# Performance work log

Measured on AMD Instinct MI355X. Metric: run time of the kernel, lower is better.

## Reference

```python
import jax, jax.numpy as jnp
import numpy as np

N = 50000      # nodes
E = 800000     # edges (avg degree 16)
F_IN = 256
F_OUT = 256


def setup_inputs() -> dict:
    key = jax.random.key(0)
    ks = jax.random.split(key, 8)
    feature = jax.random.normal(ks[0], (N, F_IN), dtype=jnp.float32)
    e_w = jax.random.uniform(ks[1], (E, 1), dtype=jnp.float32)
    snorm_n = jnp.ones((N, 1), dtype=jnp.float32)
    snorm_e = jnp.ones((E, 1), dtype=jnp.float32)
    src = jax.random.randint(ks[2], (E,), 0, N, dtype=jnp.int32)
    dst = jax.random.randint(ks[3], (E,), 0, N, dtype=jnp.int32)
    scale = 1.0 / np.sqrt(F_IN)
    W_self = jax.random.normal(ks[4], (F_IN, F_OUT), dtype=jnp.float32) * scale
    W = jax.random.normal(ks[5], (F_IN, F_OUT), dtype=jnp.float32) * scale
    b = jax.random.normal(ks[6], (F_OUT,), dtype=jnp.float32) * scale
    return {"feature": feature, "e_w": e_w, "snorm_n": snorm_n,
            "snorm_e": snorm_e, "W_self": W_self, "W": W, "b": b,
            "src": src, "dst": dst}


def reference(feature, e_w, snorm_n, snorm_e, W_self, W, b, src, dst):
    n = feature.shape[0]
    ones_e = jnp.ones_like(src, dtype=feature.dtype)
    # self transform
    h_s = feature @ W_self                                   # [N, F_OUT]
    # source-side degree normalization: deg_out^{-1/2}
    out_deg = jnp.maximum(jax.ops.segment_sum(ones_e, src, num_segments=n), 1.0)
    feat = feature * (out_deg ** -0.5)[:, None]              # [N, F_IN]
    # message = h[src] * e_w, aggregated by sum into dst (u_mul_e + sum reduce)
    msgs = feat[src] * e_w                                   # [E, F_IN]
    agg = jax.ops.segment_sum(msgs, dst, num_segments=n)     # [N, F_IN]
    # neighbor transform + destination-side degree normalization
    h = agg @ W + b                                          # [N, F_OUT]
    in_deg = jnp.maximum(jax.ops.segment_sum(ones_e, dst, num_segments=n), 1.0)
    h = h * (in_deg ** -0.5)[:, None]
    return h_s + h, e_w
```

## Files before the change

kernel.cpp:

```cpp
#include <hip/hip_runtime.h>
#include <hip/hip_bf16.h>

#define N_NODES 50000
#define N_EDGES 800000
#define MAXDEG  64

#define ROW_TILES    391
#define GEMM_BLOCKS  1564
#define EDGE_BLOCKS  782
#define TOTAL_BLOCKS 2346
#define WCONV_BLOCKS 512

typedef __bf16 bf16x8_t __attribute__((ext_vector_type(8)));
typedef float  f32x4_t  __attribute__((ext_vector_type(4)));

__device__ __forceinline__ unsigned short f2bf(float x) {
  __hip_bfloat16 h = __float2bfloat16(x);
  return __builtin_bit_cast(unsigned short, h);
}
__device__ __forceinline__ float bf2f(unsigned short u) {
  unsigned int v = ((unsigned int)u) << 16;
  return __builtin_bit_cast(float, v);
}
__device__ __forceinline__ unsigned int pk2(float lo, float hi) {
  return ((unsigned int)f2bf(hi) << 16) | (unsigned int)f2bf(lo);
}

__global__ __launch_bounds__(256) void wconv_kernel(
    const float* __restrict__ Wself, const float* __restrict__ W,
    unsigned short* __restrict__ Bt)
{
  int idx = blockIdx.x * 256 + threadIdx.x;
  int n = idx >> 8, k = idx & 255;
  float v = (n < 256) ? Wself[k * 256 + n] : W[k * 256 + (n - 256)];
  Bt[idx] = f2bf(v);
}

__global__ __launch_bounds__(256, 4) void gemm_edge_kernel(
    const float* __restrict__ feature,
    const unsigned short* __restrict__ Bt,
    const float* __restrict__ e_w, const int* __restrict__ src, const int* __restrict__ dst,
    int* __restrict__ cnt_in, int* __restrict__ cnt_out,
    unsigned int* __restrict__ bucket, float* __restrict__ out1,
    float* __restrict__ out0,
    unsigned char* __restrict__ y8)
{
  const int b   = blockIdx.x;
  const int tid = threadIdx.x;

  if (b % 3 == 2) {
    const int e0 = (b / 3) * 1024 + tid;
#pragma unroll
    for (int k = 0; k < 4; ++k) {
      int e = e0 + k * 256;
      if (e < N_EDGES) {
        int s = src[e];
        int d = dst[e];
        float w = e_w[e];
        out1[e] = w;
        atomicAdd(&cnt_out[s], 1);
        int p = atomicAdd(&cnt_in[d], 1);
        if (p < MAXDEG) {
          unsigned int ent = ((unsigned int)f2bf(w) << 16) | (unsigned int)s;
          bucket[(size_t)d * MAXDEG + p] = ent;
        }
      }
    }
    return;
  }

  __shared__ __align__(16) unsigned short As[2][128 * 32];
  __shared__ __align__(16) unsigned short Bs[2][128 * 32];

  const int g    = (b / 3) * 2 + (b % 3);
  const int q    = g & 3;
  const int m0   = (g >> 2) * 128;
  const int bn0  = q * 128;
  const int lane = tid & 63;
  const int wave = tid >> 6;
  const int wm   = (wave & 1) * 64;
  const int wn   = (wave >> 1) * 64;
  const int fr   = lane & 15;
  const int fkc  = lane >> 4;

  const int ra = tid >> 1, ha = tid & 1;
  const int sA = (ra >> 1) & 3;
  const int arow = (m0 + ra < N_NODES) ? (m0 + ra) : 0;
  const float* aptr = feature + (size_t)arow * 256;
  const int cg0 = (2 * ha) ^ sA;
  const int cg1 = (2 * ha + 1) ^ sA;
  const int aw0 = ra * 32 + (2 * ha) * 8;
  const int aw1 = aw0 + 8;

  f32x4_t acc[4][4] = {};

  {
#pragma unroll
    for (int i = 0; i < 2; ++i) {
      int r  = i * 64 + (tid >> 2);
      int cg = (tid & 3) ^ ((r >> 1) & 3);
      const unsigned short* gb = Bt + (size_t)(bn0 + r) * 256 + cg * 8;
      __builtin_amdgcn_global_load_lds((const __attribute__((address_space(1))) void*)gb,
                                       (__attribute__((address_space(3))) void*)&Bs[0][i * 2048 + wave * 512],
                                       16, 0, 0);
    }
    float4 a0 = *(const float4*)(aptr + cg0 * 8);
    float4 a1 = *(const float4*)(aptr + cg0 * 8 + 4);
    float4 a2 = *(const float4*)(aptr + cg1 * 8);
    float4 a3 = *(const float4*)(aptr + cg1 * 8 + 4);
    uint4 p0, p1;
    p0.x = pk2(a0.x, a0.y); p0.y = pk2(a0.z, a0.w);
    p0.z = pk2(a1.x, a1.y); p0.w = pk2(a1.z, a1.w);
    p1.x = pk2(a2.x, a2.y); p1.y = pk2(a2.z, a2.w);
    p1.z = pk2(a3.x, a3.y); p1.w = pk2(a3.z, a3.w);
    *(uint4*)&As[0][aw0] = p0;
    *(uint4*)&As[0][aw1] = p1;
  }
  __syncthreads();

#pragma unroll
  for (int s = 0; s < 8; ++s) {
    const int cb = s & 1, nb = cb ^ 1;
    float4 a0, a1, a2, a3;
    if (s < 7) {
      const int k0 = (s + 1) * 32;
#pragma unroll
      for (int i = 0; i < 2; ++i) {
        int r  = i * 64 + (tid >> 2);
        int cg = (tid & 3) ^ ((r >> 1) & 3);
        const unsigned short* gb = Bt + (size_t)(bn0 + r) * 256 + k0 + cg * 8;
        __builtin_amdgcn_global_load_lds((const __attribute__((address_space(1))) void*)gb,
                                         (__attribute__((address_space(3))) void*)&Bs[nb][i * 2048 + wave * 512],
                                         16, 0, 0);
      }
      a0 = *(const float4*)(aptr + k0 + cg0 * 8);
      a1 = *(const float4*)(aptr + k0 + cg0 * 8 + 4);
      a2 = *(const float4*)(aptr + k0 + cg1 * 8);
      a3 = *(const float4*)(aptr + k0 + cg1 * 8 + 4);
    }

    bf16x8_t af[4], bv[4];
#pragma unroll
    for (int i = 0; i < 4; ++i) {
      int R = wm + i * 16 + fr;
      af[i] = *(const bf16x8_t*)&As[cb][R * 32 + ((fkc ^ ((R >> 1) & 3)) * 8)];
    }
#pragma unroll
    for (int j = 0; j < 4; ++j) {
      int R = wn + j * 16 + fr;
      bv[j] = *(const bf16x8_t*)&Bs[cb][R * 32 + ((fkc ^ ((R >> 1) & 3)) * 8)];
    }
#pragma unroll
    for (int i = 0; i < 4; ++i)
#pragma unroll
      for (int j = 0; j < 4; ++j)
        acc[i][j] = __builtin_amdgcn_mfma_f32_16x16x32_bf16(af[i], bv[j], acc[i][j], 0, 0, 0);

    if (s < 7) {
      uint4 p0, p1;
      p0.x = pk2(a0.x, a0.y); p0.y = pk2(a0.z, a0.w);
      p0.z = pk2(a1.x, a1.y); p0.w = pk2(a1.z, a1.w);
      p1.x = pk2(a2.x, a2.y); p1.y = pk2(a2.z, a2.w);
      p1.z = pk2(a3.x, a3.y); p1.w = pk2(a3.z, a3.w);
      *(uint4*)&As[nb][aw0] = p0;
      *(uint4*)&As[nb][aw1] = p1;
      __syncthreads();
    }
  }

  if (q < 2) {
    const int cbase = q * 128 + wn + (lane & 15);
#pragma unroll
    for (int i = 0; i < 4; ++i) {
      int rowb = m0 + wm + i * 16 + (lane >> 4) * 4;
#pragma unroll
      for (int j = 0; j < 4; ++j) {
        int col = cbase + j * 16;
#pragma unroll
        for (int r = 0; r < 4; ++r) {
          int row = rowb + r;
          if (row < N_NODES)
            out0[(size_t)row * 256 + col] = acc[i][j][r];
        }
      }
    }
  } else {
    const int cbase = (q - 2) * 128 + wn + (lane & 15);
#pragma unroll
    for (int i = 0; i < 4; ++i) {
      int rowb = m0 + wm + i * 16 + (lane >> 4) * 4;
#pragma unroll
      for (int j = 0; j < 4; ++j) {
        int col = cbase + j * 16;
#pragma unroll
        for (int r = 0; r < 4; ++r) {
          int row = rowb + r;
          if (row < N_NODES) {
            float ys = acc[i][j][r];
            unsigned int pk = (unsigned int)__builtin_amdgcn_cvt_pk_fp8_f32(ys, ys, 0, false);
            y8[(size_t)row * 256 + col] = (unsigned char)(pk & 0xffu);
          }
        }
      }
    }
  }
}

__global__ __launch_bounds__(256) void agg_kernel(
    const unsigned char* __restrict__ y8, const unsigned int* __restrict__ bucket,
    const int* __restrict__ cnt_in, const int* __restrict__ cnt_out,
    const float* __restrict__ bias, float* __restrict__ out0)
{
  const int hw   = threadIdx.x >> 5;
  const int lane = threadIdx.x & 31;
  const int node = blockIdx.x * 8 + hw;
  if (node >= N_NODES) return;
  int deg_raw = cnt_in[node];
  int deg = deg_raw > MAXDEG ? MAXDEG : deg_raw;

  float a0 = 0.f, a1 = 0.f, a2 = 0.f, a3 = 0.f;
  float a4 = 0.f, a5 = 0.f, a6 = 0.f, a7 = 0.f;

  for (int bb = 0; bb < MAXDEG; bb += 32) {
    if (bb >= deg) break;
    int idx = bb + lane;
    unsigned int ent = (idx < deg) ? bucket[(size_t)node * MAXDEG + idx] : 0u;
    int   sl = (int)(ent & 0xffffu);
    float wl = bf2f((unsigned short)(ent >> 16));
    int co = cnt_out[sl]; if (co < 1) co = 1;
    wl *= rsqrtf((float)co);

#pragma unroll
    for (int t0 = 0; t0 < 32; t0 += 16) {
      if (bb + t0 >= deg) break;
#pragma unroll
      for (int t = 0; t < 16; ++t) {
        int eb = t0 + t;
        int   s = __shfl(sl, eb, 32);
        float w = __shfl(wl, eb, 32);
        uint2 u = *(const uint2*)(y8 + (size_t)s * 256 + lane * 8);
        a0 += w * __builtin_amdgcn_cvt_f32_fp8(u.x, 0);
        a1 += w * __builtin_amdgcn_cvt_f32_fp8(u.x, 1);
        a2 += w * __builtin_amdgcn_cvt_f32_fp8(u.x, 2);
        a3 += w * __builtin_amdgcn_cvt_f32_fp8(u.x, 3);
        a4 += w * __builtin_amdgcn_cvt_f32_fp8(u.y, 0);
        a5 += w * __builtin_amdgcn_cvt_f32_fp8(u.y, 1);
        a6 += w * __builtin_amdgcn_cvt_f32_fp8(u.y, 2);
        a7 += w * __builtin_amdgcn_cvt_f32_fp8(u.y, 3);
      }
    }
  }

  int dn = deg_raw < 1 ? 1 : deg_raw;
  float inv = rsqrtf((float)dn);
  float4 b0 = *(const float4*)(bias + lane * 8);
  float4 b1 = *(const float4*)(bias + lane * 8 + 4);
  size_t off = (size_t)node * 256 + lane * 8;
  float4 o0 = *(float4*)(out0 + off);
  float4 o1 = *(float4*)(out0 + off + 4);
  o0.x += (a0 + b0.x) * inv;  o0.y += (a1 + b0.y) * inv;
  o0.z += (a2 + b0.z) * inv;  o0.w += (a3 + b0.w) * inv;
  o1.x += (a4 + b1.x) * inv;  o1.y += (a5 + b1.y) * inv;
  o1.z += (a6 + b1.z) * inv;  o1.w += (a7 + b1.w) * inv;
  *(float4*)(out0 + off)     = o0;
  *(float4*)(out0 + off + 4) = o1;
}

extern "C" void kernel_launch(void* const* d_in, const int* in_sizes, int n_in,
                              void* d_out, int out_size, void* d_ws, size_t ws_size,
                              hipStream_t stream) {
  const float* feature = (const float*)d_in[0];
  const float* e_w     = (const float*)d_in[1];
  const float* W_self  = (const float*)d_in[4];
  const float* W       = (const float*)d_in[5];
  const float* bias    = (const float*)d_in[6];
  const int*   src     = (const int*)d_in[7];
  const int*   dst     = (const int*)d_in[8];

  float* out0 = (float*)d_out;
  float* out1 = out0 + (size_t)N_NODES * 256;

  char* ws = (char*)d_ws;
  int*            cnt_in  = (int*)(ws + 0);
  int*            cnt_out = (int*)(ws + 204800);
  unsigned int*   bucket  = (unsigned int*)(ws + 409600);
  unsigned short* Bt      = (unsigned short*)(ws + 13209600);
  unsigned char*  y8      = (unsigned char*)(ws + 13471744);

  hipMemsetAsync(ws, 0, 409600, stream);

  wconv_kernel<<<WCONV_BLOCKS, 256, 0, stream>>>(W_self, W, Bt);
  gemm_edge_kernel<<<TOTAL_BLOCKS, 256, 0, stream>>>(
      feature, Bt, e_w, src, dst, cnt_in, cnt_out, bucket, out1, out0, y8);
  agg_kernel<<<(N_NODES + 7) / 8, 256, 0, stream>>>(y8, bucket, cnt_in, cnt_out, bias, out0);
}
```

Before: 256.1 us.

## Replace fixed-capacity edge buckets with compact CSR built via counting and scan

Edge degree counting and rank assignment move into a prep kernel fused with the weight conversion. A single-block prefix scan then builds CSR offsets, and the edge blocks inside the GEMM kernel scatter packed entries into a compact CSR array instead of 64-slot per-node buckets. This shrinks the adjacency storage and the memset, and removes the MAXDEG truncation. The cost is an extra serial scan launch and an additional pass over the edges. The A-tile load addressing is also reworked so each thread reads contiguous global chunks and applies the swizzle on the LDS store side.

```diff
diff --git a/kernel.cpp b/kernel.cpp
--- a/kernel.cpp
+++ b/kernel.cpp
@@ -3,13 +3,12 @@
 
 #define N_NODES 50000
 #define N_EDGES 800000
-#define MAXDEG  64
 
 #define ROW_TILES    391
-#define GEMM_BLOCKS  1564
+#define WCONV_BLOCKS 512
 #define EDGE_BLOCKS  782
-#define TOTAL_BLOCKS 2346
-#define WCONV_BLOCKS 512
+#define K1_BLOCKS    (WCONV_BLOCKS + EDGE_BLOCKS)
+#define K3_BLOCKS    2346
 
 typedef __bf16 bf16x8_t __attribute__((ext_vector_type(8)));
 typedef float  f32x4_t  __attribute__((ext_vector_type(4)));
@@ -26,22 +25,69 @@
   return ((unsigned int)f2bf(hi) << 16) | (unsigned int)f2bf(lo);
 }
 
-__global__ __launch_bounds__(256) void wconv_kernel(
+__global__ __launch_bounds__(256) void prep_kernel(
     const float* __restrict__ Wself, const float* __restrict__ W,
-    unsigned short* __restrict__ Bt)
+    const float* __restrict__ e_w, const int* __restrict__ src, const int* __restrict__ dst,
+    unsigned short* __restrict__ Bt, int* __restrict__ cnt_in, int* __restrict__ cnt_out,
+    unsigned char* __restrict__ rank8, float* __restrict__ out1)
 {
-  int idx = blockIdx.x * 256 + threadIdx.x;
-  int n = idx >> 8, k = idx & 255;
-  float v = (n < 256) ? Wself[k * 256 + n] : W[k * 256 + (n - 256)];
-  Bt[idx] = f2bf(v);
+  const int b = blockIdx.x, tid = threadIdx.x;
+  if (b < WCONV_BLOCKS) {
+    int idx = b * 256 + tid;
+    int n = idx >> 8, k = idx & 255;
+    float v = (n < 256) ? Wself[k * 256 + n] : W[k * 256 + (n - 256)];
+    Bt[idx] = f2bf(v);
+    return;
+  }
+  const int e0 = (b - WCONV_BLOCKS) * 1024 + tid;
+#pragma unroll
+  for (int k = 0; k < 4; ++k) {
+    int e = e0 + k * 256;
+    if (e < N_EDGES) {
+      int s = src[e], d = dst[e];
+      out1[e] = e_w[e];
+      atomicAdd(&cnt_out[s], 1);
+      rank8[e] = (unsigned char)atomicAdd(&cnt_in[d], 1);
+    }
+  }
+}
+
+#define SCAN_CHUNK 49
+__global__ __launch_bounds__(1024) void scan_kernel(
+    const int* __restrict__ cnt, int* __restrict__ off)
+{
+  const int t = threadIdx.x;
+  const int c0 = t * SCAN_CHUNK;
+  int s = 0;
+#pragma unroll
+  for (int i = 0; i < SCAN_CHUNK; ++i) {
+    int idx = c0 + i;
+    s += (idx < N_NODES) ? cnt[idx] : 0;
+  }
+  __shared__ int sm[1024];
+  sm[t] = s;
+  __syncthreads();
+  for (int d = 1; d < 1024; d <<= 1) {
+    int v = (t >= d) ? sm[t - d] : 0;
+    __syncthreads();
+    sm[t] += v;
+    __syncthreads();
+  }
+  int run = sm[t] - s;
+#pragma unroll
+  for (int i = 0; i < SCAN_CHUNK; ++i) {
+    int idx = c0 + i;
+    if (idx <= N_NODES) off[idx] = run;
+    run += (idx < N_NODES) ? cnt[idx] : 0;
+  }
 }
 
 __global__ __launch_bounds__(256, 4) void gemm_edge_kernel(
     const float* __restrict__ feature,
     const unsigned short* __restrict__ Bt,
     const float* __restrict__ e_w, const int* __restrict__ src, const int* __restrict__ dst,
-    int* __restrict__ cnt_in, int* __restrict__ cnt_out,
-    unsigned int* __restrict__ bucket, float* __restrict__ out1,
+    const unsigned char* __restrict__ rank8, const int* __restrict__ off,
+    unsigned int* __restrict__ csr,
     float* __restrict__ out0,
     unsigned char* __restrict__ y8)
 {
@@ -54,16 +100,11 @@
     for (int k = 0; k < 4; ++k) {
       int e = e0 + k * 256;
       if (e < N_EDGES) {
+        int d = dst[e];
+        int r = rank8[e];
+        float w = e_w[e];
         int s = src[e];
-        int d = dst[e];
-        float w = e_w[e];
-        out1[e] = w;
-        atomicAdd(&cnt_out[s], 1);
-        int p = atomicAdd(&cnt_in[d], 1);
-        if (p < MAXDEG) {
-          unsigned int ent = ((unsigned int)f2bf(w) << 16) | (unsigned int)s;
-          bucket[(size_t)d * MAXDEG + p] = ent;
-        }
+        csr[off[d] + r] = ((unsigned int)f2bf(w) << 16) | (unsigned int)s;
       }
     }
     return;
@@ -86,11 +127,9 @@
   const int ra = tid >> 1, ha = tid & 1;
   const int sA = (ra >> 1) & 3;
   const int arow = (m0 + ra < N_NODES) ? (m0 + ra) : 0;
-  const float* aptr = feature + (size_t)arow * 256;
-  const int cg0 = (2 * ha) ^ sA;
-  const int cg1 = (2 * ha + 1) ^ sA;
-  const int aw0 = ra * 32 + (2 * ha) * 8;
-  const int aw1 = aw0 + 8;
+  const float* aptr = feature + (size_t)arow * 256 + ha * 16;
+  const int aw0 = ra * 32 + (((2 * ha) ^ sA) * 8);
+  const int aw1 = ra * 32 + ((((2 * ha) | 1) ^ sA) * 8);
 
   f32x4_t acc[4][4] = {};
 
@@ -104,10 +143,10 @@
                                        (__attribute__((address_space(3))) void*)&Bs[0][i * 2048 + wave * 512],
                                        16, 0, 0);
     }
-    float4 a0 = *(const float4*)(aptr + cg0 * 8);
-    float4 a1 = *(const float4*)(aptr + cg0 * 8 + 4);
-    float4 a2 = *(const float4*)(aptr + cg1 * 8);
-    float4 a3 = *(const float4*)(aptr + cg1 * 8 + 4);
+    float4 a0 = *(const float4*)(aptr + 0);
+    float4 a1 = *(const float4*)(aptr + 4);
+    float4 a2 = *(const float4*)(aptr + 8);
+    float4 a3 = *(const float4*)(aptr + 12);
     uint4 p0, p1;
     p0.x = pk2(a0.x, a0.y); p0.y = pk2(a0.z, a0.w);
     p0.z = pk2(a1.x, a1.y); p0.w = pk2(a1.z, a1.w);
@@ -133,10 +172,10 @@
                                          (__attribute__((address_space(3))) void*)&Bs[nb][i * 2048 + wave * 512],
                                          16, 0, 0);
       }
-      a0 = *(const float4*)(aptr + k0 + cg0 * 8);
-      a1 = *(const float4*)(aptr + k0 + cg0 * 8 + 4);
-      a2 = *(const float4*)(aptr + k0 + cg1 * 8);
-      a3 = *(const float4*)(aptr + k0 + cg1 * 8 + 4);
+      a0 = *(const float4*)(aptr + k0 + 0);
+      a1 = *(const float4*)(aptr + k0 + 4);
+      a2 = *(const float4*)(aptr + k0 + 8);
+      a3 = *(const float4*)(aptr + k0 + 12);
     }
 
     bf16x8_t af[4], bv[4];
@@ -207,24 +246,23 @@
 }
 
 __global__ __launch_bounds__(256) void agg_kernel(
-    const unsigned char* __restrict__ y8, const unsigned int* __restrict__ bucket,
-    const int* __restrict__ cnt_in, const int* __restrict__ cnt_out,
+    const unsigned char* __restrict__ y8, const unsigned int* __restrict__ csr,
+    const int* __restrict__ off, const int* __restrict__ cnt_in, const int* __restrict__ cnt_out,
     const float* __restrict__ bias, float* __restrict__ out0)
 {
   const int hw   = threadIdx.x >> 5;
   const int lane = threadIdx.x & 31;
   const int node = blockIdx.x * 8 + hw;
   if (node >= N_NODES) return;
-  int deg_raw = cnt_in[node];
-  int deg = deg_raw > MAXDEG ? MAXDEG : deg_raw;
+  const int deg  = cnt_in[node];
+  const int base = off[node];
 
   float a0 = 0.f, a1 = 0.f, a2 = 0.f, a3 = 0.f;
   float a4 = 0.f, a5 = 0.f, a6 = 0.f, a7 = 0.f;
 
-  for (int bb = 0; bb < MAXDEG; bb += 32) {
-    if (bb >= deg) break;
+  for (int bb = 0; bb < deg; bb += 32) {
     int idx = bb + lane;
-    unsigned int ent = (idx < deg) ? bucket[(size_t)node * MAXDEG + idx] : 0u;
+    unsigned int ent = (idx < deg) ? csr[base + idx] : 0u;
     int   sl = (int)(ent & 0xffffu);
     float wl = bf2f((unsigned short)(ent >> 16));
     int co = cnt_out[sl]; if (co < 1) co = 1;
@@ -251,19 +289,19 @@
     }
   }
 
-  int dn = deg_raw < 1 ? 1 : deg_raw;
+  int dn = deg < 1 ? 1 : deg;
   float inv = rsqrtf((float)dn);
   float4 b0 = *(const float4*)(bias + lane * 8);
   float4 b1 = *(const float4*)(bias + lane * 8 + 4);
-  size_t off = (size_t)node * 256 + lane * 8;
-  float4 o0 = *(float4*)(out0 + off);
-  float4 o1 = *(float4*)(out0 + off + 4);
+  size_t offo = (size_t)node * 256 + lane * 8;
+  float4 o0 = *(float4*)(out0 + offo);
+  float4 o1 = *(float4*)(out0 + offo + 4);
   o0.x += (a0 + b0.x) * inv;  o0.y += (a1 + b0.y) * inv;
   o0.z += (a2 + b0.z) * inv;  o0.w += (a3 + b0.w) * inv;
   o1.x += (a4 + b1.x) * inv;  o1.y += (a5 + b1.y) * inv;
   o1.z += (a6 + b1.z) * inv;  o1.w += (a7 + b1.w) * inv;
-  *(float4*)(out0 + off)     = o0;
-  *(float4*)(out0 + off + 4) = o1;
+  *(float4*)(out0 + offo)     = o0;
+  *(float4*)(out0 + offo + 4) = o1;
 }
 
 extern "C" void kernel_launch(void* const* d_in, const int* in_sizes, int n_in,
@@ -282,15 +320,19 @@
 
   char* ws = (char*)d_ws;
   int*            cnt_in  = (int*)(ws + 0);
-  int*            cnt_out = (int*)(ws + 204800);
-  unsigned int*   bucket  = (unsigned int*)(ws + 409600);
-  unsigned short* Bt      = (unsigned short*)(ws + 13209600);
-  unsigned char*  y8      = (unsigned char*)(ws + 13471744);
-
-  hipMemsetAsync(ws, 0, 409600, stream);
-
-  wconv_kernel<<<WCONV_BLOCKS, 256, 0, stream>>>(W_self, W, Bt);
-  gemm_edge_kernel<<<TOTAL_BLOCKS, 256, 0, stream>>>(
-      feature, Bt, e_w, src, dst, cnt_in, cnt_out, bucket, out1, out0, y8);
-  agg_kernel<<<(N_NODES + 7) / 8, 256, 0, stream>>>(y8, bucket, cnt_in, cnt_out, bias, out0);
-}
+  int*            cnt_out = (int*)(ws + 262144);
+  int*            off     = (int*)(ws + 524288);
+  unsigned char*  rank8   = (unsigned char*)(ws + 786432);
+  unsigned int*   csr     = (unsigned int*)(ws + 1835008);
+  unsigned short* Bt      = (unsigned short*)(ws + 5242880);
+  unsigned char*  y8      = (unsigned char*)(ws + 5767168);
+
+  hipMemsetAsync(ws, 0, 524288, stream);
+
+  prep_kernel<<<K1_BLOCKS, 256, 0, stream>>>(
+      W_self, W, e_w, src, dst, Bt, cnt_in, cnt_out, rank8, out1);
+  scan_kernel<<<1, 1024, 0, stream>>>(cnt_in, off);
+  gemm_edge_kernel<<<K3_BLOCKS, 256, 0, stream>>>(
+      feature, Bt, e_w, src, dst, rank8, off, csr, out0, y8);
+  agg_kernel<<<(N_NODES + 7) / 8, 256, 0, stream>>>(y8, csr, off, cnt_in, cnt_out, bias, out0);
+}
```

Measured after the change: 376.8 us. 47.2% more time.
